# Kernel optimization log

Hardware: AMD Instinct MI355X
Metric: run time of the kernel (lower is better)

The kernel has to match this reference:

```python
import jax, jax.numpy as jnp
import numpy as np

KH = KW = 3
STRIDE = 1
PAD = 1
DIL = 1


def setup_inputs() -> dict:
    key = jax.random.key(0)
    k1, k2, k3, k4 = jax.random.split(key, 4)
    B, C, H, W = 16, 64, 64, 64
    Cout = 64
    K = KH * KW
    x = jax.random.normal(k1, (B, C, H, W), jnp.float32)
    offset = jax.random.normal(k2, (B, 2 * K, H, W), jnp.float32)
    mask = jax.random.uniform(k3, (B, K, H, W), jnp.float32)
    # uniform(-stdv, stdv) init with stdv = 1/sqrt(C*KH*KW) ~ 0.0417; scaled normal is close enough
    weight = jax.random.normal(k4, (Cout, C, KH, KW), jnp.float32) * 0.04
    bias = jnp.zeros((Cout,), jnp.float32)  # no_bias=True -> frozen zeros, still added
    return dict(input=x, offset=offset, mask=mask, weight=weight, bias=bias)


def _bilinear(img, py, px):
    # img: [C, H, W]; py, px: [K, Ho, Wo] float sampling coords
    # DCNv2 semantics: out-of-bounds corner contributions are zero.
    H, W = img.shape[1], img.shape[2]
    y0f = jnp.floor(py)
    x0f = jnp.floor(px)
    wy = py - y0f
    wx = px - x0f
    y0 = y0f.astype(jnp.int32)
    x0 = x0f.astype(jnp.int32)
    out = jnp.zeros((img.shape[0],) + py.shape, img.dtype)
    for dy in (0, 1):
        for dx in (0, 1):
            yi = y0 + dy
            xi = x0 + dx
            valid = ((yi >= 0) & (yi < H) & (xi >= 0) & (xi < W)).astype(img.dtype)
            v = img[:, jnp.clip(yi, 0, H - 1), jnp.clip(xi, 0, W - 1)]  # [C,K,Ho,Wo]
            w = (wy if dy else 1.0 - wy) * (wx if dx else 1.0 - wx)
            out = out + v * (w * valid)[None]
    return out  # [C, K, Ho, Wo]


def reference(input, offset, mask, weight, bias):
    B, C, H, W = input.shape
    Cout, _, kh, kw = weight.shape
    K = kh * kw
    Ho = (H + 2 * PAD - (DIL * (kh - 1) + 1)) // STRIDE + 1
    Wo = (W + 2 * PAD - (DIL * (kw - 1) + 1)) // STRIDE + 1
    off = offset.reshape(B, K, 2, Ho, Wo)  # per kernel point: (dy, dx)
    ky = jnp.repeat(jnp.arange(kh), kw)  # [K] kernel row index
    kx = jnp.tile(jnp.arange(kw), kh)    # [K] kernel col index
    base_y = jnp.arange(Ho) * STRIDE - PAD
    base_x = jnp.arange(Wo) * STRIDE - PAD
    py = off[:, :, 0] + (base_y[None, None, :, None] + (ky * DIL)[None, :, None, None])
    px = off[:, :, 1] + (base_x[None, None, None, :] + (kx * DIL)[None, :, None, None])
    sampled = jax.vmap(_bilinear)(input, py, px)        # [B, C, K, Ho, Wo]
    modulated = sampled * mask[:, None]                 # mask-modulated accumulation
    out = jnp.einsum('bckpq,ock->bopq', modulated, weight.reshape(Cout, C, K))
    return out + bias[None, :, None, None]
```

## Files before the change

### kernel.cpp

```cpp
#include <hip/hip_runtime.h>

#define BATCH 16
#define C_IN  64
#define HH    64
#define WW    64
#define COUT  64
#define KK    9
#define HW    4096
#define CK    576
#define MROW  200

typedef __bf16 bf16x8 __attribute__((ext_vector_type(8)));
typedef float  f32x4  __attribute__((ext_vector_type(4)));

__device__ __forceinline__ unsigned int f32_to_bf16_rne(float f) {
    unsigned int b = __float_as_uint(f);
    b += 0x7FFFu + ((b >> 16) & 1u);
    return b >> 16;
}

__global__ __launch_bounds__(256) void prep_kernel(
    const float* __restrict__ x, const float* __restrict__ w,
    unsigned short* __restrict__ xt, unsigned short* __restrict__ wt) {
    __shared__ unsigned short tile[64][72];
    const int t = threadIdx.x;
    const int blk = blockIdx.x;
    if (blk < 1024) {
        const int b = blk >> 6, y = blk & 63;
        const float* xrow = x + ((b * 64) * 64 + y) * 64;
#pragma unroll
        for (int it = 0; it < 4; ++it) {
            const int idx = it * 256 + t;
            const int c = idx >> 4, seg = idx & 15;
            const float4 v = *(const float4*)(xrow + c * HW + seg * 4);
            tile[seg * 4 + 0][c] = (unsigned short)f32_to_bf16_rne(v.x);
            tile[seg * 4 + 1][c] = (unsigned short)f32_to_bf16_rne(v.y);
            tile[seg * 4 + 2][c] = (unsigned short)f32_to_bf16_rne(v.z);
            tile[seg * 4 + 3][c] = (unsigned short)f32_to_bf16_rne(v.w);
        }
        __syncthreads();
#pragma unroll
        for (int it = 0; it < 2; ++it) {
            const int idx = it * 256 + t;
            const int xx = idx >> 3, cs = idx & 7;
            *(int4*)&xt[((b * HW) + y * 64 + xx) * 64 + cs * 8] =
                *(const int4*)&tile[xx][cs * 8];
        }
    } else {
        const int i = (blk - 1024) * 256 + t;
        const int j = i & 7;
        const int l = (i >> 3) & 63;
        const int ot = (i >> 9) & 3;
        const int r = i >> 11;
        const int ks = r % 6, kc = r / 6;
        const int o  = ot * 16 + (l & 15);
        const int kk = ks * 32 + (l >> 4) * 8 + j;
        const int tap = kk >> 6, c = kk & 63;
        const int k = kc * 3 + tap;
        wt[i] = (unsigned short)f32_to_bf16_rne(w[o * CK + c * KK + k]);
    }
}

__global__ __launch_bounds__(128, 3) void dcn_main_kernel(
    const float* __restrict__ offset, const float* __restrict__ mask,
    const unsigned short* __restrict__ xt, const unsigned short* __restrict__ wt,
    const float* __restrict__ bias, float* __restrict__ out) {
    __shared__ __align__(16) unsigned short Mlds[2][16 * MROW];
    __shared__ __align__(16) int PWw[2][144 * 4];
    __shared__ __align__(8) unsigned short PWa[2][144 * 4];

    const int t    = threadIdx.x;
    const int wave = __builtin_amdgcn_readfirstlane(t >> 6);
    const int lane = t & 63;
    const int quad = lane >> 4, m16 = lane & 15;

    const int blk = blockIdx.x;
    const int xcd = blk & 7;
    const int i8  = blk >> 3;
    const int s   = ((i8 & 31) << 3) | (i8 >> 5);
    const int b   = (xcd << 1) | (s >> 7);
    const int rr  = s & 127;
    const int row = rr >> 1;
    const int qbase = (rr & 1) * 32 + wave * 16;

    f32x4 acc[4];
#pragma unroll
    for (int ot = 0; ot < 4; ++ot)
#pragma unroll
        for (int r = 0; r < 4; ++r) acc[ot][r] = 0.f;

    const float* offb = offset + b * (2 * KK * HW) + row * 64;
    const float* mb   = mask + b * (KK * HW) + row * 64;
    const char* xtb   = (const char*)(xt + b * (HW * 64));
    char* MW = (char*)Mlds[wave];
    const int co = m16 * 8;

#pragma unroll
    for (int p = 0; p < 3; ++p) {
        if (lane < 48) {
            const int t3  = lane >> 4;
            const int tap = p * 3 + t3;
            const int pxi = lane & 15;
            const int q = qbase + pxi;
            const float oy = offb[(2 * tap) * HW + q];
            const float ox = offb[(2 * tap + 1) * HW + q];
            const float mk = mb[tap * HW + q];
            const float py  = oy + (float)(row - 1 + p);
            const float pxf = ox + (float)(q - 1 + t3);
            const float y0f = floorf(py), x0f = floorf(pxf);
            const float wy = py - y0f, wx = pxf - x0f;
            const int y0 = (int)y0f, x0 = (int)x0f;
            const int y1 = y0 + 1,   x1 = x0 + 1;
            const float vy0 = (y0 >= 0 && y0 < HH) ? 1.f : 0.f;
            const float vy1 = (y1 >= 0 && y1 < HH) ? 1.f : 0.f;
            const float vx0 = (x0 >= 0 && x0 < WW) ? 1.f : 0.f;
            const float vx1 = (x1 >= 0 && x1 < WW) ? 1.f : 0.f;
            const float w00 = (1.f - wy) * (1.f - wx) * vy0 * vx0 * mk;
            const float w01 = (1.f - wy) * wx         * vy0 * vx1 * mk;
            const float w10 = wy * (1.f - wx)         * vy1 * vx0 * mk;
            const float w11 = wy * wx                 * vy1 * vx1 * mk;
            const int cy0 = min(max(y0, 0), HH - 1), cy1 = min(max(y1, 0), HH - 1);
            const int cx0 = min(max(x0, 0), WW - 1), cx1 = min(max(x1, 0), WW - 1);
            const int it = tap * 16 + pxi;
            int4 P0;
            P0.x = __float_as_int(w00); P0.y = __float_as_int(w01);
            P0.z = __float_as_int(w10); P0.w = __float_as_int(w11);
            *(int4*)&PWw[wave][it * 4] = P0;
            ushort4 A;
            A.x = (unsigned short)(cy0 * 64 + cx0);
            A.y = (unsigned short)(cy0 * 64 + cx1);
            A.z = (unsigned short)(cy1 * 64 + cx0);
            A.w = (unsigned short)(cy1 * 64 + cx1);
            *(ushort4*)&PWa[wave][it * 4] = A;
        }
    }

    uint2 g[12][4];

    auto bload = [&](int kc) {
        const unsigned short* Pa = &PWa[wave][0] + 48 * kc * 4;
#pragma unroll
        for (int i = 0; i < 12; ++i) {
            const int l = i * 4 + quad;
            const ushort4 a = *(const ushort4*)(Pa + l * 4);
            g[i][0] = *(const uint2*)(xtb + ((int)a.x << 7) + co);
            g[i][1] = *(const uint2*)(xtb + ((int)a.y << 7) + co);
            g[i][2] = *(const uint2*)(xtb + ((int)a.z << 7) + co);
            g[i][3] = *(const uint2*)(xtb + ((int)a.w << 7) + co);
        }
    };

    auto bfinish = [&](int kc) {
        const int* Pw = &PWw[wave][0] + 48 * kc * 4;
#pragma unroll
        for (int i = 0; i < 12; ++i) {
            const int l = i * 4 + quad;
            const int4 p0 = *(const int4*)(Pw + l * 4);
            const float fw00 = __int_as_float(p0.x), fw01 = __int_as_float(p0.y);
            const float fw10 = __int_as_float(p0.z), fw11 = __int_as_float(p0.w);
            const uint2 u0 = g[i][0], u1 = g[i][1], u2 = g[i][2], u3 = g[i][3];
            float v0, v1, v2, v3;
            v0 = fw00 * __uint_as_float(u0.x << 16);
            v1 = fw00 * __uint_as_float(u0.x & 0xFFFF0000u);
            v2 = fw00 * __uint_as_float(u0.y << 16);
            v3 = fw00 * __uint_as_float(u0.y & 0xFFFF0000u);
            v0 = fmaf(fw01, __uint_as_float(u1.x << 16), v0);
            v1 = fmaf(fw01, __uint_as_float(u1.x & 0xFFFF0000u), v1);
            v2 = fmaf(fw01, __uint_as_float(u1.y << 16), v2);
            v3 = fmaf(fw01, __uint_as_float(u1.y & 0xFFFF0000u), v3);
            v0 = fmaf(fw10, __uint_as_float(u2.x << 16), v0);
            v1 = fmaf(fw10, __uint_as_float(u2.x & 0xFFFF0000u), v1);
            v2 = fmaf(fw10, __uint_as_float(u2.y << 16), v2);
            v3 = fmaf(fw10, __uint_as_float(u2.y & 0xFFFF0000u), v3);
            v0 = fmaf(fw11, __uint_as_float(u3.x << 16), v0);
            v1 = fmaf(fw11, __uint_as_float(u3.x & 0xFFFF0000u), v1);
            v2 = fmaf(fw11, __uint_as_float(u3.y << 16), v2);
            v3 = fmaf(fw11, __uint_as_float(u3.y & 0xFFFF0000u), v3);
            uint2 pk;
            pk.x = (f32_to_bf16_rne(v1) << 16) | f32_to_bf16_rne(v0);
            pk.y = (f32_to_bf16_rne(v3) << 16) | f32_to_bf16_rne(v2);
            *(uint2*)(MW + (l & 15) * 400 + (l >> 4) * 128 + m16 * 8) = pk;
        }
    };

    auto phaseC = [&](int kc) {
        const unsigned short* wkc = wt + kc * (6 * 4 * 512);
#pragma unroll
        for (int ks = 0; ks < 6; ++ks) {
            const bf16x8 bfrag =
                *(const bf16x8*)(MW + m16 * 400 + ks * 64 + quad * 16);
#pragma unroll
            for (int ot = 0; ot < 4; ++ot) {
                const bf16x8 afrag =
                    *(const bf16x8*)(wkc + (ks * 4 + ot) * 512 + lane * 8);
                acc[ot] = __builtin_amdgcn_mfma_f32_16x16x32_bf16(afrag, bfrag,
                                                                  acc[ot], 0, 0, 0);
            }
        }
    };

    bload(0);
    __builtin_amdgcn_sched_barrier(0);
    for (int kc = 0; kc < 3; ++kc) {
        bfinish(kc);
        if (kc < 2) {
            bload(kc + 1);
            __builtin_amdgcn_sched_barrier(0);
        }
        phaseC(kc);
    }

    float* ob = out + b * (COUT * HW) + row * 64 + qbase + m16;
#pragma unroll
    for (int ot = 0; ot < 4; ++ot)
#pragma unroll
        for (int r = 0; r < 4; ++r) {
            const int o = ot * 16 + quad * 4 + r;
            ob[o * HW] = acc[ot][r] + bias[o];
        }
}

extern "C" void kernel_launch(void* const* d_in, const int* in_sizes, int n_in,
                              void* d_out, int out_size, void* d_ws,
                              size_t ws_size, hipStream_t stream) {
    const float* x    = (const float*)d_in[0];
    const float* off  = (const float*)d_in[1];
    const float* mask = (const float*)d_in[2];
    const float* w    = (const float*)d_in[3];
    const float* bias = (const float*)d_in[4];
    float* out = (float*)d_out;

    unsigned short* xt = (unsigned short*)d_ws;
    unsigned short* wt = (unsigned short*)((char*)d_ws + 8388608);

    prep_kernel<<<1024 + 144, 256, 0, stream>>>(x, w, xt, wt);
    dcn_main_kernel<<<2048, 128, 0, stream>>>(off, mask, xt, wt, bias, out);
}
```

Measured before the change: 115.5 us.

## Switch gather/interp path to fp16 packed math with wider loads

Converts the transposed input, the weights and the bilinear coefficients to fp16 instead of bf16. The bilinear interpolation now runs as packed half2 FMAs rather than unpacking bf16 to fp32 and repacking with manual rounding, and the MFMA switches to the f16 variant. Each lane now gathers 16-byte chunks covering 8 channels instead of 8-byte chunks, halving the loop count and the number of gather instructions. Launch bounds are raised to 4 blocks per SU for occupancy. The cost is that fp16 has less range than bf16 and interpolation is accumulated in half precision, which may affect accuracy.

```diff
diff --git a/kernel.cpp b/kernel.cpp
--- a/kernel.cpp
+++ b/kernel.cpp
@@ -1,4 +1,5 @@
 #include <hip/hip_runtime.h>
+#include <hip/hip_fp16.h>
 
 #define BATCH 16
 #define C_IN  64
@@ -10,13 +11,21 @@
 #define CK    576
 #define MROW  200
 
-typedef __bf16 bf16x8 __attribute__((ext_vector_type(8)));
-typedef float  f32x4  __attribute__((ext_vector_type(4)));
-
-__device__ __forceinline__ unsigned int f32_to_bf16_rne(float f) {
-    unsigned int b = __float_as_uint(f);
-    b += 0x7FFFu + ((b >> 16) & 1u);
-    return b >> 16;
+typedef _Float16 f16x8 __attribute__((ext_vector_type(8)));
+typedef float    f32x4 __attribute__((ext_vector_type(4)));
+
+__device__ __forceinline__ unsigned short f32_to_f16u(float f) {
+    _Float16 h = (_Float16)f;
+    unsigned short u;
+    __builtin_memcpy(&u, &h, 2);
+    return u;
+}
+
+__device__ __forceinline__ __half2 as_h2(unsigned int u) {
+    __half2 r; __builtin_memcpy(&r, &u, 4); return r;
+}
+__device__ __forceinline__ unsigned int as_u32(__half2 v) {
+    unsigned int u; __builtin_memcpy(&u, &v, 4); return u;
 }
 
 __global__ __launch_bounds__(256) void prep_kernel(
@@ -33,10 +42,10 @@
             const int idx = it * 256 + t;
             const int c = idx >> 4, seg = idx & 15;
             const float4 v = *(const float4*)(xrow + c * HW + seg * 4);
-            tile[seg * 4 + 0][c] = (unsigned short)f32_to_bf16_rne(v.x);
-            tile[seg * 4 + 1][c] = (unsigned short)f32_to_bf16_rne(v.y);
-            tile[seg * 4 + 2][c] = (unsigned short)f32_to_bf16_rne(v.z);
-            tile[seg * 4 + 3][c] = (unsigned short)f32_to_bf16_rne(v.w);
+            tile[seg * 4 + 0][c] = f32_to_f16u(v.x);
+            tile[seg * 4 + 1][c] = f32_to_f16u(v.y);
+            tile[seg * 4 + 2][c] = f32_to_f16u(v.z);
+            tile[seg * 4 + 3][c] = f32_to_f16u(v.w);
         }
         __syncthreads();
 #pragma unroll
@@ -57,11 +66,11 @@
         const int kk = ks * 32 + (l >> 4) * 8 + j;
         const int tap = kk >> 6, c = kk & 63;
         const int k = kc * 3 + tap;
-        wt[i] = (unsigned short)f32_to_bf16_rne(w[o * CK + c * KK + k]);
+        wt[i] = f32_to_f16u(w[o * CK + c * KK + k]);
     }
 }
 
-__global__ __launch_bounds__(128, 3) void dcn_main_kernel(
+__global__ __launch_bounds__(128, 4) void dcn_main_kernel(
     const float* __restrict__ offset, const float* __restrict__ mask,
     const unsigned short* __restrict__ xt, const unsigned short* __restrict__ wt,
     const float* __restrict__ bias, float* __restrict__ out) {
@@ -93,7 +102,8 @@
     const float* mb   = mask + b * (KK * HW) + row * 64;
     const char* xtb   = (const char*)(xt + b * (HW * 64));
     char* MW = (char*)Mlds[wave];
-    const int co = m16 * 8;
+    const int lg  = lane >> 3;
+    const int co2 = (lane & 7) * 16;
 
 #pragma unroll
     for (int p = 0; p < 3; ++p) {
@@ -122,9 +132,15 @@
             const int cy0 = min(max(y0, 0), HH - 1), cy1 = min(max(y1, 0), HH - 1);
             const int cx0 = min(max(x0, 0), WW - 1), cx1 = min(max(x1, 0), WW - 1);
             const int it = tap * 16 + pxi;
+            const unsigned int s00 = f32_to_f16u(w00);
+            const unsigned int s01 = f32_to_f16u(w01);
+            const unsigned int s10 = f32_to_f16u(w10);
+            const unsigned int s11 = f32_to_f16u(w11);
             int4 P0;
-            P0.x = __float_as_int(w00); P0.y = __float_as_int(w01);
-            P0.z = __float_as_int(w10); P0.w = __float_as_int(w11);
+            P0.x = (int)(s00 | (s00 << 16));
+            P0.y = (int)(s01 | (s01 << 16));
+            P0.z = (int)(s10 | (s10 << 16));
+            P0.w = (int)(s11 | (s11 << 16));
             *(int4*)&PWw[wave][it * 4] = P0;
             ushort4 A;
             A.x = (unsigned short)(cy0 * 64 + cx0);
@@ -135,51 +151,62 @@
         }
     }
 
-    uint2 g[12][4];
+    uint4 g[6][4];
 
     auto bload = [&](int kc) {
         const unsigned short* Pa = &PWa[wave][0] + 48 * kc * 4;
 #pragma unroll
-        for (int i = 0; i < 12; ++i) {
-            const int l = i * 4 + quad;
+        for (int i = 0; i < 6; ++i) {
+            const int l = i * 8 + lg;
             const ushort4 a = *(const ushort4*)(Pa + l * 4);
-            g[i][0] = *(const uint2*)(xtb + ((int)a.x << 7) + co);
-            g[i][1] = *(const uint2*)(xtb + ((int)a.y << 7) + co);
-            g[i][2] = *(const uint2*)(xtb + ((int)a.z << 7) + co);
-            g[i][3] = *(const uint2*)(xtb + ((int)a.w << 7) + co);
+            g[i][0] = *(const uint4*)(xtb + ((int)a.x << 7) + co2);
+            g[i][1] = *(const uint4*)(xtb + ((int)a.y << 7) + co2);
+            g[i][2] = *(const uint4*)(xtb + ((int)a.z << 7) + co2);
+            g[i][3] = *(const uint4*)(xtb + ((int)a.w << 7) + co2);
         }
     };
 
     auto bfinish = [&](int kc) {
         const int* Pw = &PWw[wave][0] + 48 * kc * 4;
 #pragma unroll
-        for (int i = 0; i < 12; ++i) {
-            const int l = i * 4 + quad;
+        for (int i = 0; i < 6; ++i) {
+            const int l = i * 8 + lg;
             const int4 p0 = *(const int4*)(Pw + l * 4);
-            const float fw00 = __int_as_float(p0.x), fw01 = __int_as_float(p0.y);
-            const float fw10 = __int_as_float(p0.z), fw11 = __int_as_float(p0.w);
-            const uint2 u0 = g[i][0], u1 = g[i][1], u2 = g[i][2], u3 = g[i][3];
-            float v0, v1, v2, v3;
-            v0 = fw00 * __uint_as_float(u0.x << 16);
-            v1 = fw00 * __uint_as_float(u0.x & 0xFFFF0000u);
-            v2 = fw00 * __uint_as_float(u0.y << 16);
-            v3 = fw00 * __uint_as_float(u0.y & 0xFFFF0000u);
-            v0 = fmaf(fw01, __uint_as_float(u1.x << 16), v0);
-            v1 = fmaf(fw01, __uint_as_float(u1.x & 0xFFFF0000u), v1);
-            v2 = fmaf(fw01, __uint_as_float(u1.y << 16), v2);
-            v3 = fmaf(fw01, __uint_as_float(u1.y & 0xFFFF0000u), v3);
-            v0 = fmaf(fw10, __uint_as_float(u2.x << 16), v0);
-            v1 = fmaf(fw10, __uint_as_float(u2.x & 0xFFFF0000u), v1);
-            v2 = fmaf(fw10, __uint_as_float(u2.y << 16), v2);
-            v3 = fmaf(fw10, __uint_as_float(u2.y & 0xFFFF0000u), v3);
-            v0 = fmaf(fw11, __uint_as_float(u3.x << 16), v0);
-            v1 = fmaf(fw11, __uint_as_float(u3.x & 0xFFFF0000u), v1);
-            v2 = fmaf(fw11, __uint_as_float(u3.y << 16), v2);
-            v3 = fmaf(fw11, __uint_as_float(u3.y & 0xFFFF0000u), v3);
-            uint2 pk;
-            pk.x = (f32_to_bf16_rne(v1) << 16) | f32_to_bf16_rne(v0);
-            pk.y = (f32_to_bf16_rne(v3) << 16) | f32_to_bf16_rne(v2);
-            *(uint2*)(MW + (l & 15) * 400 + (l >> 4) * 128 + m16 * 8) = pk;
+            const __half2 c00 = as_h2((unsigned)p0.x);
+            const __half2 c01 = as_h2((unsigned)p0.y);
+            const __half2 c10 = as_h2((unsigned)p0.z);
+            const __half2 c11 = as_h2((unsigned)p0.w);
+            const uint4 q0 = g[i][0], q1 = g[i][1], q2 = g[i][2], q3 = g[i][3];
+            uint4 ov;
+            {
+                __half2 v = __hmul2(c00, as_h2(q0.x));
+                v = __hfma2(c01, as_h2(q1.x), v);
+                v = __hfma2(c10, as_h2(q2.x), v);
+                v = __hfma2(c11, as_h2(q3.x), v);
+                ov.x = as_u32(v);
+            }
+            {
+                __half2 v = __hmul2(c00, as_h2(q0.y));
+                v = __hfma2(c01, as_h2(q1.y), v);
+                v = __hfma2(c10, as_h2(q2.y), v);
+                v = __hfma2(c11, as_h2(q3.y), v);
+                ov.y = as_u32(v);
+            }
+            {
+                __half2 v = __hmul2(c00, as_h2(q0.z));
+                v = __hfma2(c01, as_h2(q1.z), v);
+                v = __hfma2(c10, as_h2(q2.z), v);
+                v = __hfma2(c11, as_h2(q3.z), v);
+                ov.z = as_u32(v);
+            }
+            {
+                __half2 v = __hmul2(c00, as_h2(q0.w));
+                v = __hfma2(c01, as_h2(q1.w), v);
+                v = __hfma2(c10, as_h2(q2.w), v);
+                v = __hfma2(c11, as_h2(q3.w), v);
+                ov.w = as_u32(v);
+            }
+            *(uint4*)(MW + (l & 15) * 400 + (l >> 4) * 128 + co2) = ov;
         }
     };
 
@@ -187,14 +214,14 @@
         const unsigned short* wkc = wt + kc * (6 * 4 * 512);
 #pragma unroll
         for (int ks = 0; ks < 6; ++ks) {
-            const bf16x8 bfrag =
-                *(const bf16x8*)(MW + m16 * 400 + ks * 64 + quad * 16);
+            const f16x8 bfrag =
+                *(const f16x8*)(MW + m16 * 400 + ks * 64 + quad * 16);
 #pragma unroll
             for (int ot = 0; ot < 4; ++ot) {
-                const bf16x8 afrag =
-                    *(const bf16x8*)(wkc + (ks * 4 + ot) * 512 + lane * 8);
-                acc[ot] = __builtin_amdgcn_mfma_f32_16x16x32_bf16(afrag, bfrag,
-                                                                  acc[ot], 0, 0, 0);
+                const f16x8 afrag =
+                    *(const f16x8*)(wkc + (ks * 4 + ot) * 512 + lane * 8);
+                acc[ot] = __builtin_amdgcn_mfma_f32_16x16x32_f16(afrag, bfrag,
+                                                                 acc[ot], 0, 0, 0);
             }
         }
     };
```

Measured after the change: 108.2 us. 6.3% less time.
